# Kernel tuning notes

Measured on AMD Instinct MI355X. Metric: run time of the kernel, lower is better.

The kernel has to match this reference:

```python
import jax, jax.numpy as jnp
import numpy as np

N = 2048
D = 128
E = 16384
NEG = -9e15


def setup_inputs() -> dict:
    key = jax.random.key(0)
    k1, k2, k3, k4, k5 = jax.random.split(key, 5)
    X_n = jax.random.normal(k1, (N, D), dtype=jnp.float32)
    edge_indices = jax.random.randint(k2, (2, E), 0, N, dtype=jnp.int64)
    adj = jax.random.randint(k3, (N, N), 0, 2, dtype=jnp.int32)
    W1 = jax.random.normal(k4, (D, D), dtype=jnp.float32) * (2.0 / D) ** 0.5
    W2 = jax.random.normal(k5, (1, 2 * D), dtype=jnp.float32) * (1.0 / D) ** 0.5
    return {"X_n": X_n, "edge_indices": edge_indices, "adj": adj, "W1": W1, "W2": W2}


def reference(X_n, edge_indices, adj, W1, W2):
    # f_w1: identity-activation Linear without bias -> X_n @ W1.T  [N, D]
    Xw = X_n @ W1.T
    d = Xw.shape[1]
    # f_w2 on concat(Xw[i], Xw[j]) decomposes into two rank-1 score vectors:
    # weight[i, j] = Xw[i] . W2[0, :d] + Xw[j] . W2[0, d:]
    s_i = Xw @ W2[0, :d]   # [N]
    s_j = Xw @ W2[0, d:]   # [N]
    weight = s_i[:, None] + s_j[None, :]            # [N, N]
    masked = jnp.where(adj > 0, weight, jnp.float32(NEG))
    attention = jax.nn.softmax(masked, axis=1)       # [N, N]
    src, dst = edge_indices[0], edge_indices[1]
    a_p = attention[dst, src]                        # [E]
    a_c = attention[src, dst]                        # [E]
    e = edge_indices.shape[1]
    cols = jnp.arange(e)
    atten_matrix = jnp.zeros((X_n.shape[0], 2 * e), dtype=jnp.float32)
    atten_matrix = atten_matrix.at[dst, cols].set(a_p)
    atten_matrix = atten_matrix.at[src, cols + e].set(a_c)
    return atten_matrix
```

## Files before the change

### kernel.cpp

```cpp
#include <hip/hip_runtime.h>

#define NN 2048
#define DD 128
#define EE 16384

typedef float v4f __attribute__((ext_vector_type(4)));
typedef int   v4i __attribute__((ext_vector_type(4)));

__global__ void k_sj(const float* __restrict__ X, const float* __restrict__ W1,
                     const float* __restrict__ W2, float* __restrict__ ev) {
    __shared__ float u[DD];
    const int t = threadIdx.x;
    if (t < DD) {
        float acc = 0.f;
#pragma unroll 8
        for (int k = 0; k < DD; ++k) acc += W2[DD + k] * W1[k * DD + t];
        u[t] = acc;
    }
    __syncthreads();
    const int wave = t >> 6, lane = t & 63;
    const int row0 = blockIdx.x * 16 + wave * 4;
#pragma unroll
    for (int rr = 0; rr < 4; ++rr) {
        const int row = row0 + rr;
        const float2 v = ((const float2*)(X + (size_t)row * DD))[lane];
        float acc = v.x * u[2 * lane] + v.y * u[2 * lane + 1];
#pragma unroll
        for (int off = 32; off; off >>= 1) acc += __shfl_down(acc, off);
        if (lane == 0) ev[row] = expf(acc);
    }
}

__global__ void k_rowz(const int* __restrict__ adj, const float* __restrict__ ev,
                       float* __restrict__ Zv) {
    const int i = blockIdx.x;
    const int t = threadIdx.x;
    const int4* arow = (const int4*)(adj + (size_t)i * NN);
    const float4* ef = (const float4*)ev;
    float acc = 0.f;
#pragma unroll
    for (int b = 0; b < NN / 4; b += 256) {
        const int4   a  = arow[b + t];
        const float4 e4 = ef[b + t];
        acc += (float)a.x * e4.x + (float)a.y * e4.y +
               (float)a.z * e4.z + (float)a.w * e4.w;
    }
#pragma unroll
    for (int off = 32; off; off >>= 1) acc += __shfl_down(acc, off);
    __shared__ float wsum[4];
    if ((t & 63) == 0) wsum[t >> 6] = acc;
    __syncthreads();
    if (t == 0) Zv[i] = wsum[0] + wsum[1] + wsum[2] + wsum[3];
}

__global__ void k_vals(const int* __restrict__ ei, const int* __restrict__ adj,
                       const float* __restrict__ ev, const float* __restrict__ Zv,
                       int* __restrict__ rowid, float* __restrict__ val) {
    const int e = blockIdx.x * blockDim.x + threadIdx.x;
    if (e >= EE) return;
    const int s = ei[e];
    const int d = ei[EE + e];
    const float invn = 1.0f / (float)NN;

    const float zd = Zv[d];
    float ap;
    if (zd == 0.f) ap = invn;
    else ap = (adj[(size_t)d * NN + s] > 0) ? ev[s] / zd : 0.f;

    const float zs = Zv[s];
    float ac;
    if (zs == 0.f) ac = invn;
    else ac = (adj[(size_t)s * NN + d] > 0) ? ev[d] / zs : 0.f;

    rowid[e]      = d;  val[e]      = ap;
    rowid[EE + e] = s;  val[EE + e] = ac;
}

__global__ __launch_bounds__(256) void k_write(const int* __restrict__ rowid,
                                               const float* __restrict__ val,
                                               v4f* __restrict__ out4) {
    const int l  = blockIdx.x * 256 + threadIdx.x;
    const int r  = l >> 13;
    const int c4 = l & 8191;
    const v4i rid = ((const v4i*)rowid)[c4];
    const v4f vv  = ((const v4f*)val)[c4];
    v4f o;
    o.x = (rid.x == r) ? vv.x : 0.f;
    o.y = (rid.y == r) ? vv.y : 0.f;
    o.z = (rid.z == r) ? vv.z : 0.f;
    o.w = (rid.w == r) ? vv.w : 0.f;
    __builtin_nontemporal_store(o, out4 + l);
}

extern "C" void kernel_launch(void* const* d_in, const int* in_sizes, int n_in,
                              void* d_out, int out_size, void* d_ws, size_t ws_size,
                              hipStream_t stream) {
    const float* X   = (const float*)d_in[0];
    const int*   ei  = (const int*)d_in[1];
    const int*   adj = (const int*)d_in[2];
    const float* W1  = (const float*)d_in[3];
    const float* W2  = (const float*)d_in[4];

    float* ev    = (float*)d_ws;
    float* Zv    = ev + NN;
    float* val   = Zv + NN;
    int*   rowid = (int*)(val + 2 * EE);

    k_sj   <<<NN / 16,  256, 0, stream>>>(X, W1, W2, ev);
    k_rowz <<<NN,       256, 0, stream>>>(adj, ev, Zv);
    k_vals <<<EE / 256, 256, 0, stream>>>(ei, adj, ev, Zv, rowid, val);

    const int n4 = out_size / 4;
    k_write<<<n4 / 256, 256, 0, stream>>>(rowid, val, (v4f*)d_out);
}
```

Baseline: 295.5 us.

## Fuse output zeroing into row-sum kernel and scatter edge values directly

After: 311.7 us. 1.05x slower.

```diff
diff --git a/kernel.cpp b/kernel.cpp
--- a/kernel.cpp
+++ b/kernel.cpp
@@ -3,9 +3,9 @@
 #define NN 2048
 #define DD 128
 #define EE 16384
+#define TWOE (2 * EE)
 
 typedef float v4f __attribute__((ext_vector_type(4)));
-typedef int   v4i __attribute__((ext_vector_type(4)));
 
 __global__ void k_sj(const float* __restrict__ X, const float* __restrict__ W1,
                      const float* __restrict__ W2, float* __restrict__ ev) {
@@ -31,12 +31,15 @@
     }
 }
 
-__global__ void k_rowz(const int* __restrict__ adj, const float* __restrict__ ev,
-                       float* __restrict__ Zv) {
+__global__ __launch_bounds__(256) void k_zero_z(const int* __restrict__ adj,
+                                                const float* __restrict__ ev,
+                                                float* __restrict__ Zv,
+                                                float* __restrict__ out) {
     const int i = blockIdx.x;
     const int t = threadIdx.x;
-    const int4* arow = (const int4*)(adj + (size_t)i * NN);
-    const float4* ef = (const float4*)ev;
+
+    const int4*   arow = (const int4*)(adj + (size_t)i * NN);
+    const float4* ef   = (const float4*)ev;
     float acc = 0.f;
 #pragma unroll
     for (int b = 0; b < NN / 4; b += 256) {
@@ -45,6 +48,13 @@
         acc += (float)a.x * e4.x + (float)a.y * e4.y +
                (float)a.z * e4.z + (float)a.w * e4.w;
     }
+
+    v4f z4 = {0.f, 0.f, 0.f, 0.f};
+    v4f* orow = (v4f*)(out + (size_t)i * TWOE);
+#pragma unroll
+    for (int b = 0; b < TWOE / 4; b += 256)
+        orow[b + t] = z4;
+
 #pragma unroll
     for (int off = 32; off; off >>= 1) acc += __shfl_down(acc, off);
     __shared__ float wsum[4];
@@ -53,9 +63,9 @@
     if (t == 0) Zv[i] = wsum[0] + wsum[1] + wsum[2] + wsum[3];
 }
 
-__global__ void k_vals(const int* __restrict__ ei, const int* __restrict__ adj,
-                       const float* __restrict__ ev, const float* __restrict__ Zv,
-                       int* __restrict__ rowid, float* __restrict__ val) {
+__global__ void k_scatter(const int* __restrict__ ei, const int* __restrict__ adj,
+                          const float* __restrict__ ev, const float* __restrict__ Zv,
+                          float* __restrict__ out) {
     const int e = blockIdx.x * blockDim.x + threadIdx.x;
     if (e >= EE) return;
     const int s = ei[e];
@@ -72,24 +82,8 @@
     if (zs == 0.f) ac = invn;
     else ac = (adj[(size_t)s * NN + d] > 0) ? ev[d] / zs : 0.f;
 
-    rowid[e]      = d;  val[e]      = ap;
-    rowid[EE + e] = s;  val[EE + e] = ac;
-}
-
-__global__ __launch_bounds__(256) void k_write(const int* __restrict__ rowid,
-                                               const float* __restrict__ val,
-                                               v4f* __restrict__ out4) {
-    const int l  = blockIdx.x * 256 + threadIdx.x;
-    const int r  = l >> 13;
-    const int c4 = l & 8191;
-    const v4i rid = ((const v4i*)rowid)[c4];
-    const v4f vv  = ((const v4f*)val)[c4];
-    v4f o;
-    o.x = (rid.x == r) ? vv.x : 0.f;
-    o.y = (rid.y == r) ? vv.y : 0.f;
-    o.z = (rid.z == r) ? vv.z : 0.f;
-    o.w = (rid.w == r) ? vv.w : 0.f;
-    __builtin_nontemporal_store(o, out4 + l);
+    out[(size_t)d * TWOE + e]      = ap;
+    out[(size_t)s * TWOE + EE + e] = ac;
 }
 
 extern "C" void kernel_launch(void* const* d_in, const int* in_sizes, int n_in,
@@ -101,15 +95,12 @@
     const float* W1  = (const float*)d_in[3];
     const float* W2  = (const float*)d_in[4];
 
-    float* ev    = (float*)d_ws;
-    float* Zv    = ev + NN;
-    float* val   = Zv + NN;
-    int*   rowid = (int*)(val + 2 * EE);
+    float* ev = (float*)d_ws;
+    float* Zv = ev + NN;
 
-    k_sj   <<<NN / 16,  256, 0, stream>>>(X, W1, W2, ev);
-    k_rowz <<<NN,       256, 0, stream>>>(adj, ev, Zv);
-    k_vals <<<EE / 256, 256, 0, stream>>>(ei, adj, ev, Zv, rowid, val);
+    float* out = (float*)d_out;
 
-    const int n4 = out_size / 4;
-    k_write<<<n4 / 256, 256, 0, stream>>>(rowid, val, (v4f*)d_out);
+    k_sj      <<<NN / 16,  256, 0, stream>>>(X, W1, W2, ev);
+    k_zero_z  <<<NN,       256, 0, stream>>>(adj, ev, Zv, out);
+    k_scatter <<<EE / 256, 256, 0, stream>>>(ei, adj, ev, Zv, out);
 }
```
